# Optimization experiments

Measured on AMD Instinct MI355X. Metric: run time of the kernel, lower is better.

## Reference

```python
import jax, jax.numpy as jnp
import numpy as np

INPUT_DIM = 100
LATENT_DIM = 128
HIDDEN_DIM = 64
BATCH = 16384


def setup_inputs() -> dict:
    key = jax.random.key(0)
    ku, k1, kb1, k2, kb2 = jax.random.split(key, 5)
    u = jax.random.normal(ku, (BATCH, INPUT_DIM), dtype=jnp.float32)
    # PyTorch Linear init: U(-1/sqrt(fan_in), 1/sqrt(fan_in))
    s1 = 1.0 / np.sqrt(INPUT_DIM)
    s2 = 1.0 / np.sqrt(HIDDEN_DIM)
    W1 = jax.random.uniform(k1, (LATENT_DIM, HIDDEN_DIM, INPUT_DIM), jnp.float32, -s1, s1)
    b1 = jax.random.uniform(kb1, (LATENT_DIM, HIDDEN_DIM), jnp.float32, -s1, s1)
    W2 = jax.random.uniform(k2, (LATENT_DIM, HIDDEN_DIM), jnp.float32, -s2, s2)  # out_features=1 squeezed
    b2 = jax.random.uniform(kb2, (LATENT_DIM,), jnp.float32, -s2, s2)
    return {"u": u, "W1": W1, "b1": b1, "W2": W2, "b2": b2}


def reference(u, W1, b1, W2, b2):
    # All latent_dim branches batched as one grouped GEMM.
    # h: [batch, latent, hidden]
    h = jnp.tanh(jnp.einsum('bi,khi->bkh', u, W1) + b1[None, :, :])
    # out: [batch, latent]  (second Linear has output dim 1, squeezed)
    out = jnp.einsum('bkh,kh->bk', h, W2) + b2[None, :]
    return out
```

## Files before the change

### kernel.cpp

```cpp
#include <hip/hip_runtime.h>

#define BATCH 16384
#define LATENT 128
#define HIDDEN 64
#define INDIM 100
#define KPAD 128
#define TANH_SCALE 2.885390081777927f

typedef short shortx8 __attribute__((ext_vector_type(8)));
typedef float floatx4 __attribute__((ext_vector_type(4)));

__device__ __forceinline__ short f2bf(float f) {
    union { float f; unsigned u; } v; v.f = f;
    unsigned r = v.u + 0x7FFF + ((v.u >> 16) & 1);
    return (short)(r >> 16);
}

#if __has_builtin(__builtin_amdgcn_exp2f)
#define EXP2F(x) __builtin_amdgcn_exp2f(x)
#else
#define EXP2F(x) __exp2f(x)
#endif
#if __has_builtin(__builtin_amdgcn_rcpf)
#define RCPF(x) __builtin_amdgcn_rcpf(x)
#else
#define RCPF(x) (1.0f / (x))
#endif

#define N_U_CHUNKS (BATCH * KPAD / 8)
#define N_W_CHUNKS (LATENT * HIDDEN * KPAD / 8)

__global__ __launch_bounds__(256) void prep_all(const float* __restrict__ u,
                                                const float* __restrict__ W1,
                                                const float* __restrict__ b1,
                                                const float* __restrict__ W2,
                                                const float* __restrict__ b2,
                                                shortx8* __restrict__ uf,
                                                shortx8* __restrict__ wf,
                                                float* __restrict__ b2eff) {
    int c = blockIdx.x * 256 + threadIdx.x;
    if (c < N_U_CHUNKS) {
        int lane = c & 63;
        int kt = (c >> 6) & 3;
        int g = c >> 8;
        int row = g * 16 + (lane & 15);
        int kbase = kt * 32 + ((lane >> 4) << 3);
        shortx8 v;
        if (kbase + 7 < INDIM) {
            const float4* p = (const float4*)(u + row * INDIM + kbase);
            float4 f0 = p[0], f1 = p[1];
            v[0] = f2bf(f0.x); v[1] = f2bf(f0.y); v[2] = f2bf(f0.z); v[3] = f2bf(f0.w);
            v[4] = f2bf(f1.x); v[5] = f2bf(f1.y); v[6] = f2bf(f1.z); v[7] = f2bf(f1.w);
        } else {
#pragma unroll
            for (int j = 0; j < 8; j++) {
                int k = kbase + j;
                float f = (k < INDIM) ? u[row * INDIM + k] : (k == INDIM ? 1.0f : 0.0f);
                v[j] = f2bf(f);
            }
        }
        uf[c] = v;
    } else if (c < N_U_CHUNKS + N_W_CHUNKS) {
        int c2 = c - N_U_CHUNKS;
        int lane = c2 & 63;
        int kt = (c2 >> 6) & 3;
        int nt = (c2 >> 8) & 3;
        int lat = c2 >> 10;
        int h = nt * 16 + (lane & 15);
        int hw = lat * HIDDEN + h;
        int kbase = kt * 32 + ((lane >> 4) << 3);
        shortx8 v;
        if (kbase + 7 < INDIM) {
            const float4* p = (const float4*)(W1 + hw * INDIM + kbase);
            float4 f0 = p[0], f1 = p[1];
            v[0] = f2bf(f0.x * TANH_SCALE); v[1] = f2bf(f0.y * TANH_SCALE);
            v[2] = f2bf(f0.z * TANH_SCALE); v[3] = f2bf(f0.w * TANH_SCALE);
            v[4] = f2bf(f1.x * TANH_SCALE); v[5] = f2bf(f1.y * TANH_SCALE);
            v[6] = f2bf(f1.z * TANH_SCALE); v[7] = f2bf(f1.w * TANH_SCALE);
        } else {
#pragma unroll
            for (int j = 0; j < 8; j++) {
                int k = kbase + j;
                float f = (k < INDIM) ? W1[hw * INDIM + k] * TANH_SCALE
                                      : (k == INDIM ? b1[hw] * TANH_SCALE : 0.0f);
                v[j] = f2bf(f);
            }
        }
        wf[c2] = v;
    } else {
        int lat = c - (N_U_CHUNKS + N_W_CHUNKS);
        if (lat < LATENT) {
            float s = b2[lat];
            const float* wp = W2 + lat * HIDDEN;
#pragma unroll 8
            for (int h = 0; h < HIDDEN; h++) s += wp[h];
            b2eff[lat] = s;
        }
    }
}

__global__ __launch_bounds__(256) __attribute__((amdgpu_waves_per_eu(5, 8)))
void branch_mlp(const shortx8* __restrict__ uf,
                const shortx8* __restrict__ wf,
                const float* __restrict__ W2,
                const float* __restrict__ b2eff,
                float* __restrict__ out) {
    int tid = threadIdx.x;
    int lane = tid & 63;
    int w = tid >> 6;
    int bx = blockIdx.x;
    int lat = bx >> 5;
    int G0 = (bx & 31) * 32 + w * 8;
    int q = lane >> 4;

    __shared__ shortx8 awf[16 * 64];
    __shared__ float w2s[2][HIDDEN];

    {
        const shortx8* src = wf + (size_t)lat * 16 * 64;
#pragma unroll
        for (int j = 0; j < 4; j++) awf[j * 256 + tid] = src[j * 256 + tid];
    }
    if (tid < 128) w2s[tid >> 6][tid & 63] = -2.0f * W2[lat * HIDDEN + (tid & 63)];

    float b2v = b2eff[lat];
    __syncthreads();

    const shortx8* ua = uf + (size_t)G0 * 4 * 64 + lane;
    float* outp = out + (size_t)G0 * 16 * LATENT + lat;

#pragma unroll
    for (int g = 0; g < 8; g++) {
        int lnx = lane;
        asm volatile("" : "+v"(lnx));

        shortx8 ub[4];
#pragma unroll
        for (int kt = 0; kt < 4; kt++)
            ub[kt] = ua[(g * 4 + kt) * 64];

        floatx4 acc[4] = {};
#pragma unroll
        for (int kt = 0; kt < 4; kt++) {
            shortx8 a0 = awf[(0 + kt) * 64 + lnx];
            shortx8 a1 = awf[(4 + kt) * 64 + lnx];
            shortx8 a2 = awf[(8 + kt) * 64 + lnx];
            shortx8 a3 = awf[(12 + kt) * 64 + lnx];
            acc[0] = __builtin_amdgcn_mfma_f32_16x16x32_bf16(a0, ub[kt], acc[0], 0, 0, 0);
            acc[1] = __builtin_amdgcn_mfma_f32_16x16x32_bf16(a1, ub[kt], acc[1], 0, 0, 0);
            acc[2] = __builtin_amdgcn_mfma_f32_16x16x32_bf16(a2, ub[kt], acc[2], 0, 0, 0);
            acc[3] = __builtin_amdgcn_mfma_f32_16x16x32_bf16(a3, ub[kt], acc[3], 0, 0, 0);
        }

        float s = 0.0f;
#pragma unroll
        for (int nt = 0; nt < 4; nt++) {
            float4 wv = *(const float4*)(&w2s[g & 1][nt * 16 + q * 4]);
            float p0 = EXP2F(acc[nt][0]) + 1.0f;
            float p1 = EXP2F(acc[nt][1]) + 1.0f;
            float p2 = EXP2F(acc[nt][2]) + 1.0f;
            float p3 = EXP2F(acc[nt][3]) + 1.0f;
            float m01 = p0 * p1, m23 = p2 * p3;
            float n01 = fmaf(wv.x, p1, wv.y * p0);
            float n23 = fmaf(wv.z, p3, wv.w * p2);
            float n = fmaf(n01, m23, n23 * m01);
            s = fmaf(n, RCPF(m01 * m23), s);
        }
        s += __shfl_xor(s, 16, 64);
        s += __shfl_xor(s, 32, 64);
        if (lane < 16)
            outp[(g * 16 + lane) * LATENT] = s + b2v;
    }
}

__global__ __launch_bounds__(256) void fallback_kernel(const float* __restrict__ u, const float* __restrict__ W1,
                                                       const float* __restrict__ b1, const float* __restrict__ W2,
                                                       const float* __restrict__ b2, float* __restrict__ out) {
    int idx = blockIdx.x * 256 + threadIdx.x;
    if (idx >= BATCH * LATENT) return;
    int b = idx >> 7;
    int lat = idx & 127;
    const float* ub = u + b * INDIM;
    float s = 0.0f;
    for (int h = 0; h < HIDDEN; h++) {
        const float* wp = W1 + (lat * HIDDEN + h) * INDIM;
        float dd = b1[lat * HIDDEN + h];
        for (int k = 0; k < INDIM; k++) dd += ub[k] * wp[k];
        s += tanhf(dd) * W2[lat * HIDDEN + h];
    }
    out[idx] = s + b2[lat];
}

extern "C" void kernel_launch(void* const* d_in, const int* in_sizes, int n_in,
                              void* d_out, int out_size, void* d_ws, size_t ws_size,
                              hipStream_t stream) {
    const float* u  = (const float*)d_in[0];
    const float* W1 = (const float*)d_in[1];
    const float* b1 = (const float*)d_in[2];
    const float* W2 = (const float*)d_in[3];
    const float* b2 = (const float*)d_in[4];
    float* out = (float*)d_out;

    const size_t UF_BYTES = (size_t)BATCH * KPAD * 2;
    const size_t WF_BYTES = (size_t)LATENT * HIDDEN * KPAD * 2;
    const size_t B2_BYTES = LATENT * sizeof(float);

    if (ws_size < UF_BYTES + WF_BYTES + B2_BYTES) {
        fallback_kernel<<<(BATCH * LATENT + 255) / 256, 256, 0, stream>>>(u, W1, b1, W2, b2, out);
        return;
    }

    shortx8* uf = (shortx8*)d_ws;
    shortx8* wf = (shortx8*)((char*)d_ws + UF_BYTES);
    float* b2eff = (float*)((char*)d_ws + UF_BYTES + WF_BYTES);

    prep_all<<<(N_U_CHUNKS + N_W_CHUNKS) / 256 + 1, 256, 0, stream>>>(u, W1, b1, W2, b2, uf, wf, b2eff);
    branch_mlp<<<4096, 256, 0, stream>>>(uf, wf, W2, b2eff, out);
}
```

Baseline: 113.8 us.

## Switch grouped GEMM to 32x32x16 bf16 MFMA tiles with matching layout

Moves the main kernel from 16x16x32 MFMA instructions to 32x32x16 ones. The prep kernel now packs u and W1 into a 32-row, 16-wide K-chunk fragment layout, and the tanh/W2 epilogue is remapped to the 32x32 accumulator layout. The larger tile needs fewer MFMA issues per FLOP, fewer LDS A-fragment reads per output, and one fewer cross-lane shuffle. In exchange each thread holds 16-wide accumulators, so register pressure rises, which is why the wave occupancy hint was lowered.

```diff
diff --git a/kernel.cpp b/kernel.cpp
--- a/kernel.cpp
+++ b/kernel.cpp
@@ -9,6 +9,7 @@
 
 typedef short shortx8 __attribute__((ext_vector_type(8)));
 typedef float floatx4 __attribute__((ext_vector_type(4)));
+typedef float floatx16 __attribute__((ext_vector_type(16)));
 
 __device__ __forceinline__ short f2bf(float f) {
     union { float f; unsigned u; } v; v.f = f;
@@ -41,10 +42,10 @@
     int c = blockIdx.x * 256 + threadIdx.x;
     if (c < N_U_CHUNKS) {
         int lane = c & 63;
-        int kt = (c >> 6) & 3;
-        int g = c >> 8;
-        int row = g * 16 + (lane & 15);
-        int kbase = kt * 32 + ((lane >> 4) << 3);
+        int kt = (c >> 6) & 7;
+        int gg = c >> 9;
+        int row = gg * 32 + (lane & 31);
+        int kbase = kt * 16 + ((lane >> 5) << 3);
         shortx8 v;
         if (kbase + 7 < INDIM) {
             const float4* p = (const float4*)(u + row * INDIM + kbase);
@@ -63,12 +64,12 @@
     } else if (c < N_U_CHUNKS + N_W_CHUNKS) {
         int c2 = c - N_U_CHUNKS;
         int lane = c2 & 63;
-        int kt = (c2 >> 6) & 3;
-        int nt = (c2 >> 8) & 3;
+        int kt = (c2 >> 6) & 7;
+        int ht = (c2 >> 9) & 1;
         int lat = c2 >> 10;
-        int h = nt * 16 + (lane & 15);
+        int h = ht * 32 + (lane & 31);
         int hw = lat * HIDDEN + h;
-        int kbase = kt * 32 + ((lane >> 4) << 3);
+        int kbase = kt * 16 + ((lane >> 5) << 3);
         shortx8 v;
         if (kbase + 7 < INDIM) {
             const float4* p = (const float4*)(W1 + hw * INDIM + kbase);
@@ -99,7 +100,7 @@
     }
 }
 
-__global__ __launch_bounds__(256) __attribute__((amdgpu_waves_per_eu(5, 8)))
+__global__ __launch_bounds__(256) __attribute__((amdgpu_waves_per_eu(4, 8)))
 void branch_mlp(const shortx8* __restrict__ uf,
                 const shortx8* __restrict__ wf,
                 const float* __restrict__ W2,
@@ -110,8 +111,7 @@
     int w = tid >> 6;
     int bx = blockIdx.x;
     int lat = bx >> 5;
-    int G0 = (bx & 31) * 32 + w * 8;
-    int q = lane >> 4;
+    int G0 = (bx & 31) * 16 + w * 4;
 
     __shared__ shortx8 awf[16 * 64];
     __shared__ float w2s[2][HIDDEN];
@@ -126,50 +126,56 @@
     float b2v = b2eff[lat];
     __syncthreads();
 
-    const shortx8* ua = uf + (size_t)G0 * 4 * 64 + lane;
-    float* outp = out + (size_t)G0 * 16 * LATENT + lat;
-
-#pragma unroll
-    for (int g = 0; g < 8; g++) {
+    const shortx8* ua = uf + (size_t)G0 * 512 + lane;
+    float* outp = out + (size_t)G0 * 32 * LATENT + lat;
+    int l5q = (lane >> 5) << 2;
+
+    floatx16 z = {};
+
+#pragma unroll
+    for (int g = 0; g < 4; g++) {
         int lnx = lane;
         asm volatile("" : "+v"(lnx));
 
-        shortx8 ub[4];
-#pragma unroll
-        for (int kt = 0; kt < 4; kt++)
-            ub[kt] = ua[(g * 4 + kt) * 64];
-
-        floatx4 acc[4] = {};
-#pragma unroll
-        for (int kt = 0; kt < 4; kt++) {
-            shortx8 a0 = awf[(0 + kt) * 64 + lnx];
-            shortx8 a1 = awf[(4 + kt) * 64 + lnx];
-            shortx8 a2 = awf[(8 + kt) * 64 + lnx];
-            shortx8 a3 = awf[(12 + kt) * 64 + lnx];
-            acc[0] = __builtin_amdgcn_mfma_f32_16x16x32_bf16(a0, ub[kt], acc[0], 0, 0, 0);
-            acc[1] = __builtin_amdgcn_mfma_f32_16x16x32_bf16(a1, ub[kt], acc[1], 0, 0, 0);
-            acc[2] = __builtin_amdgcn_mfma_f32_16x16x32_bf16(a2, ub[kt], acc[2], 0, 0, 0);
-            acc[3] = __builtin_amdgcn_mfma_f32_16x16x32_bf16(a3, ub[kt], acc[3], 0, 0, 0);
+        shortx8 ub[8];
+#pragma unroll
+        for (int kt = 0; kt < 8; kt++)
+            ub[kt] = ua[g * 512 + kt * 64];
+
+        floatx16 acc[2];
+        {
+            shortx8 a0 = awf[0 * 64 + lnx];
+            shortx8 a1 = awf[8 * 64 + lnx];
+            acc[0] = __builtin_amdgcn_mfma_f32_32x32x16_bf16(a0, ub[0], z, 0, 0, 0);
+            acc[1] = __builtin_amdgcn_mfma_f32_32x32x16_bf16(a1, ub[0], z, 0, 0, 0);
+        }
+#pragma unroll
+        for (int kt = 1; kt < 8; kt++) {
+            shortx8 a0 = awf[kt * 64 + lnx];
+            shortx8 a1 = awf[(8 + kt) * 64 + lnx];
+            acc[0] = __builtin_amdgcn_mfma_f32_32x32x16_bf16(a0, ub[kt], acc[0], 0, 0, 0);
+            acc[1] = __builtin_amdgcn_mfma_f32_32x32x16_bf16(a1, ub[kt], acc[1], 0, 0, 0);
         }
 
         float s = 0.0f;
 #pragma unroll
-        for (int nt = 0; nt < 4; nt++) {
-            float4 wv = *(const float4*)(&w2s[g & 1][nt * 16 + q * 4]);
-            float p0 = EXP2F(acc[nt][0]) + 1.0f;
-            float p1 = EXP2F(acc[nt][1]) + 1.0f;
-            float p2 = EXP2F(acc[nt][2]) + 1.0f;
-            float p3 = EXP2F(acc[nt][3]) + 1.0f;
-            float m01 = p0 * p1, m23 = p2 * p3;
-            float n01 = fmaf(wv.x, p1, wv.y * p0);
-            float n23 = fmaf(wv.z, p3, wv.w * p2);
-            float n = fmaf(n01, m23, n23 * m01);
-            s = fmaf(n, RCPF(m01 * m23), s);
-        }
-        s += __shfl_xor(s, 16, 64);
+        for (int ht = 0; ht < 2; ht++)
+#pragma unroll
+            for (int b = 0; b < 4; b++) {
+                float4 wv = *(const float4*)(&w2s[g & 1][ht * 32 + b * 8 + l5q]);
+                float p0 = EXP2F(acc[ht][b * 4 + 0]) + 1.0f;
+                float p1 = EXP2F(acc[ht][b * 4 + 1]) + 1.0f;
+                float p2 = EXP2F(acc[ht][b * 4 + 2]) + 1.0f;
+                float p3 = EXP2F(acc[ht][b * 4 + 3]) + 1.0f;
+                float m01 = p0 * p1, m23 = p2 * p3;
+                float n01 = fmaf(wv.x, p1, wv.y * p0);
+                float n23 = fmaf(wv.z, p3, wv.w * p2);
+                float n = fmaf(n01, m23, n23 * m01);
+                s = fmaf(n, RCPF(m01 * m23), s);
+            }
         s += __shfl_xor(s, 32, 64);
-        if (lane < 16)
-            outp[(g * 16 + lane) * LATENT] = s + b2v;
+        if (lane < 32)
+            outp[(g * 32 + lane) * LATENT] = s + b2v;
     }
 }
 
```

New measurement: 114.4 us. Within noise of the previous version (+0.6%).
